# Performance work log

Hardware: AMD Instinct MI355X
Metric: run time of the kernel (lower is better)

Reference implementation:

```python
import jax, jax.numpy as jnp
import numpy as np


def setup_inputs() -> dict:
    key = jax.random.key(0)
    k1, k2, k3, k4 = jax.random.split(key, 4)
    N, E, DIN, DOUT = 16384, 8192, 128, 128
    x = jax.random.normal(k1, (N, DIN), dtype=jnp.float32)
    # sparse binary incidence matrix, avg node degree ~ E * 0.005 ~ 41
    H = (jax.random.uniform(k2, (N, E)) < 0.005).astype(jnp.float32)
    W = jax.random.normal(k3, (DOUT, DIN), dtype=jnp.float32) * (1.0 / np.sqrt(DIN))
    b = jax.random.normal(k4, (DOUT,), dtype=jnp.float32) * 0.01
    return {"x": x, "H": H, "W": W, "b": b}


def reference(x, H, W, b):
    # Degree vectors. Original builds dense diag matrices; off-diagonal zeros
    # raised to negative powers become inf and are zeroed by nan_to_num, so the
    # math reduces to elementwise inverse powers of the degree vectors with
    # non-finite entries mapped to 0.
    deg_node = jnp.sum(H, axis=1)                    # [N]
    deg_edge = jnp.sum(H, axis=0)                    # [E]
    dvih = jnp.where(deg_node > 0, deg_node ** -0.5, 0.0)   # D_v^{-1/2}
    dei = jnp.where(deg_edge > 0, 1.0 / deg_edge, 0.0)      # D_e^{-1}
    # D_v^{-1/2} H D_e^{-1} H^T D_v^{-1/2} x, as broadcasted row scalings
    y = dvih[:, None] * x                            # [N, DIN]
    y = H.T @ y                                      # [E, DIN]
    y = dei[:, None] * y                             # [E, DIN]
    y = H @ y                                        # [N, DIN]
    y = dvih[:, None] * y                            # [N, DIN]
    return y @ W.T + b                               # [N, DOUT]
```

## Files before the change

kernel.cpp:

```cpp
#include <hip/hip_runtime.h>
#include <hip/hip_bf16.h>

#define NN 16384
#define EE 8192
#define DD 128
#define CSR_STRIDE 128
#define CSC_STRIDE 192


__global__ __launch_bounds__(256) void g_gemm(
    const float* __restrict__ x,
    const float* __restrict__ W,
    float* __restrict__ xw,
    int* __restrict__ edge_cnt)
{
    const int t = threadIdx.x;
    {
        int tid = blockIdx.x * 256 + t;
        if (tid < EE) edge_cnt[tid] = 0;
    }

    __shared__ float sA[32 * 132];
    __shared__ float sW[64 * 132];
    const int m0 = blockIdx.x * 32;

#pragma unroll
    for (int r = 0; r < 16; ++r) {
        int i = t + 256 * r;
        int row = i >> 7, col = i & 127;
        sA[row * 132 + col] = x[(size_t)(m0 + row) * DD + col];
    }

    const int jg = t & 15;
    const int mg = t >> 4;
    const int m2 = mg * 2;
    const int j4 = jg * 4;

    for (int h = 0; h < 2; ++h) {
        __syncthreads();
#pragma unroll
        for (int r = 0; r < 32; ++r) {
            int i = t + 256 * r;
            int row = i >> 7, col = i & 127;
            sW[row * 132 + col] = W[(size_t)(h * 64 + row) * DD + col];
        }
        __syncthreads();

        float acc0[4] = {0.f, 0.f, 0.f, 0.f};
        float acc1[4] = {0.f, 0.f, 0.f, 0.f};
#pragma unroll 4
        for (int k = 0; k < 128; k += 4) {
            float4 a0 = *(const float4*)&sA[m2 * 132 + k];
            float4 a1 = *(const float4*)&sA[(m2 + 1) * 132 + k];
#pragma unroll
            for (int jj = 0; jj < 4; ++jj) {
                float4 w = *(const float4*)&sW[(j4 + jj) * 132 + k];
                acc0[jj] += a0.x*w.x + a0.y*w.y + a0.z*w.z + a0.w*w.w;
                acc1[jj] += a1.x*w.x + a1.y*w.y + a1.z*w.z + a1.w*w.w;
            }
        }
#pragma unroll
        for (int jj = 0; jj < 4; ++jj) {
            xw[(size_t)(m0 + m2)     * DD + h * 64 + j4 + jj] = acc0[jj];
            xw[(size_t)(m0 + m2 + 1) * DD + h * 64 + j4 + jj] = acc1[jj];
        }
    }
}

__global__ __launch_bounds__(256) void k1_parse(
    const float* __restrict__ H,
    float* __restrict__ dvih,
    int* __restrict__ csr_cnt,
    int* __restrict__ csr_idx,
    int* __restrict__ edge_cnt,
    int* __restrict__ csc_idx)
{
    const int n = blockIdx.x;
    const int t = threadIdx.x;
    __shared__ int s_cnt;
    __shared__ int s_list[CSR_STRIDE];
    if (t == 0) s_cnt = 0;
    __syncthreads();

    const float4* row = (const float4*)(H + (size_t)n * EE);
#pragma unroll
    for (int j = 0; j < 8; ++j) {
        int idx = t + 256 * j;
        float4 v = row[idx];
        int base = idx * 4;
        if (v.x != 0.0f) { int p = atomicAdd(&s_cnt, 1); if (p < CSR_STRIDE) s_list[p] = base + 0; }
        if (v.y != 0.0f) { int p = atomicAdd(&s_cnt, 1); if (p < CSR_STRIDE) s_list[p] = base + 1; }
        if (v.z != 0.0f) { int p = atomicAdd(&s_cnt, 1); if (p < CSR_STRIDE) s_list[p] = base + 2; }
        if (v.w != 0.0f) { int p = atomicAdd(&s_cnt, 1); if (p < CSR_STRIDE) s_list[p] = base + 3; }
    }
    __syncthreads();

    int cnt = s_cnt; if (cnt > CSR_STRIDE) cnt = CSR_STRIDE;
    if (t < cnt) {
        int e = s_list[t];
        csr_idx[(size_t)n * CSR_STRIDE + t] = e;
        int pos = atomicAdd(&edge_cnt[e], 1);
        if (pos < CSC_STRIDE) csc_idx[(size_t)e * CSC_STRIDE + pos] = n;
    }
    if (t == 0) {
        csr_cnt[n] = cnt;
        dvih[n] = (cnt > 0) ? (1.0f / sqrtf((float)cnt)) : 0.0f;
    }
}

__global__ __launch_bounds__(128) void k2_edge_gather(
    const float* __restrict__ xw,
    const float* __restrict__ dvih,
    const int* __restrict__ edge_cnt,
    const int* __restrict__ csc_idx,
    float* __restrict__ y2)
{
    const int e = blockIdx.x;
    const int t = threadIdx.x;
    __shared__ int   s_lst[CSC_STRIDE];
    __shared__ float s_dv[CSC_STRIDE];

    int cnt = edge_cnt[e];
    int ccnt = cnt > CSC_STRIDE ? CSC_STRIDE : cnt;
    for (int i = t; i < ccnt; i += 128) {
        int n = csc_idx[(size_t)e * CSC_STRIDE + i];
        s_lst[i] = n;
        s_dv[i]  = dvih[n];
    }
    __syncthreads();

    float s = 0.0f;
    int i = 0;
    for (; i + 8 <= ccnt; i += 8) {
        float partial = 0.0f;
#pragma unroll
        for (int u = 0; u < 8; ++u) {
            partial += s_dv[i + u] * xw[(size_t)s_lst[i + u] * DD + t];
        }
        s += partial;
    }
    for (; i < ccnt; ++i) s += s_dv[i] * xw[(size_t)s_lst[i] * DD + t];

    float dei = (cnt > 0) ? (1.0f / (float)cnt) : 0.0f;
    y2[(size_t)e * DD + t] = s * dei;
}

__global__ __launch_bounds__(128) void k3_node_gather(
    const float* __restrict__ y2,
    const float* __restrict__ dvih,
    const int* __restrict__ csr_cnt,
    const int* __restrict__ csr_idx,
    const float* __restrict__ b,
    float* __restrict__ out)
{
    const int n = blockIdx.x;
    const int t = threadIdx.x;
    __shared__ int s_lst[CSR_STRIDE];

    int cnt = csr_cnt[n];
    if (t < cnt) s_lst[t] = csr_idx[(size_t)n * CSR_STRIDE + t];
    __syncthreads();

    float s = 0.0f;
    int i = 0;
    for (; i + 8 <= cnt; i += 8) {
        float partial = 0.0f;
#pragma unroll
        for (int u = 0; u < 8; ++u) {
            partial += y2[(size_t)s_lst[i + u] * DD + t];
        }
        s += partial;
    }
    for (; i < cnt; ++i) s += y2[(size_t)s_lst[i] * DD + t];

    out[(size_t)n * DD + t] = dvih[n] * s + b[t];
}

extern "C" void kernel_launch(void* const* d_in, const int* in_sizes, int n_in,
                              void* d_out, int out_size, void* d_ws, size_t ws_size,
                              hipStream_t stream) {
    const float* x = (const float*)d_in[0];
    const float* H = (const float*)d_in[1];
    const float* W = (const float*)d_in[2];
    const float* b = (const float*)d_in[3];
    float* out = (float*)d_out;

    char* ws = (char*)d_ws;
    float* dvih    = (float*)(ws + 0);
    int*   csr_cnt = (int*)  (ws + 65536);
    int*   edge_cnt= (int*)  (ws + 131072);
    int*   csr_idx = (int*)  (ws + 163840);
    int*   csc_idx = (int*)  (ws + 8552448);
    float* xw      = (float*)(ws + 14843904);
    float* y2      = (float*)(ws + 23232512);

    g_gemm<<<NN / 32, 256, 0, stream>>>(x, W, xw, edge_cnt);
    k1_parse<<<NN, 256, 0, stream>>>(H, dvih, csr_cnt, csr_idx, edge_cnt, csc_idx);
    k2_edge_gather<<<EE, 128, 0, stream>>>(xw, dvih, edge_cnt, csc_idx, y2);
    k3_node_gather<<<NN, 128, 0, stream>>>(y2, dvih, csr_cnt, csr_idx, b, out);
}
```

Baseline: 767.4 us.

## Fuse GEMM into H-parse kernel, nontemporal H loads, two rows per gather block

The x·W GEMM and the H incidence parse now run in one launch, with blocks branching on block index so the GEMM work overlaps the bandwidth-bound scan of H. The edge_cnt zeroing moves to a memset. H rows are read with nontemporal loads to avoid polluting cache. The edge and node gather kernels now handle two rows per 256-thread block. The fused kernel needs the larger shared-memory footprint for every block, which may lower occupancy for the parse blocks.

```diff
diff --git a/kernel.cpp b/kernel.cpp
--- a/kernel.cpp
+++ b/kernel.cpp
@@ -6,126 +6,124 @@
 #define DD 128
 #define CSR_STRIDE 128
 #define CSC_STRIDE 192
-
-
-__global__ __launch_bounds__(256) void g_gemm(
+#define GEMM_BLOCKS 512
+
+typedef float f4 __attribute__((ext_vector_type(4)));
+
+
+__global__ __launch_bounds__(256) void k1_fused(
+    const float* __restrict__ H,
     const float* __restrict__ x,
     const float* __restrict__ W,
     float* __restrict__ xw,
-    int* __restrict__ edge_cnt)
-{
-    const int t = threadIdx.x;
-    {
-        int tid = blockIdx.x * 256 + t;
-        if (tid < EE) edge_cnt[tid] = 0;
-    }
-
-    __shared__ float sA[32 * 132];
-    __shared__ float sW[64 * 132];
-    const int m0 = blockIdx.x * 32;
-
-#pragma unroll
-    for (int r = 0; r < 16; ++r) {
-        int i = t + 256 * r;
-        int row = i >> 7, col = i & 127;
-        sA[row * 132 + col] = x[(size_t)(m0 + row) * DD + col];
-    }
-
-    const int jg = t & 15;
-    const int mg = t >> 4;
-    const int m2 = mg * 2;
-    const int j4 = jg * 4;
-
-    for (int h = 0; h < 2; ++h) {
-        __syncthreads();
-#pragma unroll
-        for (int r = 0; r < 32; ++r) {
-            int i = t + 256 * r;
-            int row = i >> 7, col = i & 127;
-            sW[row * 132 + col] = W[(size_t)(h * 64 + row) * DD + col];
-        }
-        __syncthreads();
-
-        float acc0[4] = {0.f, 0.f, 0.f, 0.f};
-        float acc1[4] = {0.f, 0.f, 0.f, 0.f};
-#pragma unroll 4
-        for (int k = 0; k < 128; k += 4) {
-            float4 a0 = *(const float4*)&sA[m2 * 132 + k];
-            float4 a1 = *(const float4*)&sA[(m2 + 1) * 132 + k];
-#pragma unroll
-            for (int jj = 0; jj < 4; ++jj) {
-                float4 w = *(const float4*)&sW[(j4 + jj) * 132 + k];
-                acc0[jj] += a0.x*w.x + a0.y*w.y + a0.z*w.z + a0.w*w.w;
-                acc1[jj] += a1.x*w.x + a1.y*w.y + a1.z*w.z + a1.w*w.w;
-            }
-        }
-#pragma unroll
-        for (int jj = 0; jj < 4; ++jj) {
-            xw[(size_t)(m0 + m2)     * DD + h * 64 + j4 + jj] = acc0[jj];
-            xw[(size_t)(m0 + m2 + 1) * DD + h * 64 + j4 + jj] = acc1[jj];
-        }
-    }
-}
-
-__global__ __launch_bounds__(256) void k1_parse(
-    const float* __restrict__ H,
     float* __restrict__ dvih,
     int* __restrict__ csr_cnt,
     int* __restrict__ csr_idx,
     int* __restrict__ edge_cnt,
     int* __restrict__ csc_idx)
 {
-    const int n = blockIdx.x;
+    __shared__ float smem[32 * 132 + 64 * 132];
     const int t = threadIdx.x;
-    __shared__ int s_cnt;
-    __shared__ int s_list[CSR_STRIDE];
-    if (t == 0) s_cnt = 0;
-    __syncthreads();
-
-    const float4* row = (const float4*)(H + (size_t)n * EE);
-#pragma unroll
-    for (int j = 0; j < 8; ++j) {
-        int idx = t + 256 * j;
-        float4 v = row[idx];
-        int base = idx * 4;
-        if (v.x != 0.0f) { int p = atomicAdd(&s_cnt, 1); if (p < CSR_STRIDE) s_list[p] = base + 0; }
-        if (v.y != 0.0f) { int p = atomicAdd(&s_cnt, 1); if (p < CSR_STRIDE) s_list[p] = base + 1; }
-        if (v.z != 0.0f) { int p = atomicAdd(&s_cnt, 1); if (p < CSR_STRIDE) s_list[p] = base + 2; }
-        if (v.w != 0.0f) { int p = atomicAdd(&s_cnt, 1); if (p < CSR_STRIDE) s_list[p] = base + 3; }
-    }
-    __syncthreads();
-
-    int cnt = s_cnt; if (cnt > CSR_STRIDE) cnt = CSR_STRIDE;
-    if (t < cnt) {
-        int e = s_list[t];
-        csr_idx[(size_t)n * CSR_STRIDE + t] = e;
-        int pos = atomicAdd(&edge_cnt[e], 1);
-        if (pos < CSC_STRIDE) csc_idx[(size_t)e * CSC_STRIDE + pos] = n;
-    }
-    if (t == 0) {
-        csr_cnt[n] = cnt;
-        dvih[n] = (cnt > 0) ? (1.0f / sqrtf((float)cnt)) : 0.0f;
-    }
-}
-
-__global__ __launch_bounds__(128) void k2_edge_gather(
+
+    if (blockIdx.x < GEMM_BLOCKS) {
+        float* sA = smem;
+        float* sW = smem + 32 * 132;
+        const int m0 = blockIdx.x * 32;
+
+#pragma unroll
+        for (int r = 0; r < 16; ++r) {
+            int i = t + 256 * r;
+            int row = i >> 7, col = i & 127;
+            sA[row * 132 + col] = x[(size_t)(m0 + row) * DD + col];
+        }
+
+        const int jg = t & 15;
+        const int mg = t >> 4;
+        const int m2 = mg * 2;
+        const int j4 = jg * 4;
+
+        for (int h = 0; h < 2; ++h) {
+            __syncthreads();
+#pragma unroll
+            for (int r = 0; r < 32; ++r) {
+                int i = t + 256 * r;
+                int row = i >> 7, col = i & 127;
+                sW[row * 132 + col] = W[(size_t)(h * 64 + row) * DD + col];
+            }
+            __syncthreads();
+
+            float acc0[4] = {0.f, 0.f, 0.f, 0.f};
+            float acc1[4] = {0.f, 0.f, 0.f, 0.f};
+#pragma unroll 4
+            for (int k = 0; k < 128; k += 4) {
+                float4 a0 = *(const float4*)&sA[m2 * 132 + k];
+                float4 a1 = *(const float4*)&sA[(m2 + 1) * 132 + k];
+#pragma unroll
+                for (int jj = 0; jj < 4; ++jj) {
+                    float4 w = *(const float4*)&sW[(j4 + jj) * 132 + k];
+                    acc0[jj] += a0.x*w.x + a0.y*w.y + a0.z*w.z + a0.w*w.w;
+                    acc1[jj] += a1.x*w.x + a1.y*w.y + a1.z*w.z + a1.w*w.w;
+                }
+            }
+#pragma unroll
+            for (int jj = 0; jj < 4; ++jj) {
+                xw[(size_t)(m0 + m2)     * DD + h * 64 + j4 + jj] = acc0[jj];
+                xw[(size_t)(m0 + m2 + 1) * DD + h * 64 + j4 + jj] = acc1[jj];
+            }
+        }
+    } else {
+        const int n = blockIdx.x - GEMM_BLOCKS;
+        int* s_cnt  = (int*)smem;
+        int* s_list = (int*)smem + 4;
+        if (t == 0) *s_cnt = 0;
+        __syncthreads();
+
+        const f4* row = (const f4*)(H + (size_t)n * EE);
+#pragma unroll
+        for (int j = 0; j < 8; ++j) {
+            int idx = t + 256 * j;
+            f4 v = __builtin_nontemporal_load(row + idx);
+            int base = idx * 4;
+            if (v.x != 0.0f) { int p = atomicAdd(s_cnt, 1); if (p < CSR_STRIDE) s_list[p] = base + 0; }
+            if (v.y != 0.0f) { int p = atomicAdd(s_cnt, 1); if (p < CSR_STRIDE) s_list[p] = base + 1; }
+            if (v.z != 0.0f) { int p = atomicAdd(s_cnt, 1); if (p < CSR_STRIDE) s_list[p] = base + 2; }
+            if (v.w != 0.0f) { int p = atomicAdd(s_cnt, 1); if (p < CSR_STRIDE) s_list[p] = base + 3; }
+        }
+        __syncthreads();
+
+        int cnt = *s_cnt; if (cnt > CSR_STRIDE) cnt = CSR_STRIDE;
+        if (t < cnt) {
+            int e = s_list[t];
+            csr_idx[(size_t)n * CSR_STRIDE + t] = e;
+            int pos = atomicAdd(&edge_cnt[e], 1);
+            if (pos < CSC_STRIDE) csc_idx[(size_t)e * CSC_STRIDE + pos] = n;
+        }
+        if (t == 0) {
+            csr_cnt[n] = cnt;
+            dvih[n] = (cnt > 0) ? (1.0f / sqrtf((float)cnt)) : 0.0f;
+        }
+    }
+}
+
+__global__ __launch_bounds__(256) void k2_edge_gather(
     const float* __restrict__ xw,
     const float* __restrict__ dvih,
     const int* __restrict__ edge_cnt,
     const int* __restrict__ csc_idx,
     float* __restrict__ y2)
 {
-    const int e = blockIdx.x;
-    const int t = threadIdx.x;
-    __shared__ int   s_lst[CSC_STRIDE];
-    __shared__ float s_dv[CSC_STRIDE];
+    const int sub = threadIdx.x >> 7;
+    const int t   = threadIdx.x & 127;
+    const int e   = blockIdx.x * 2 + sub;
+    __shared__ int   s_lst[2][CSC_STRIDE];
+    __shared__ float s_dv[2][CSC_STRIDE];
 
     int cnt = edge_cnt[e];
     int ccnt = cnt > CSC_STRIDE ? CSC_STRIDE : cnt;
     for (int i = t; i < ccnt; i += 128) {
         int n = csc_idx[(size_t)e * CSC_STRIDE + i];
-        s_lst[i] = n;
-        s_dv[i]  = dvih[n];
+        s_lst[sub][i] = n;
+        s_dv[sub][i]  = dvih[n];
     }
     __syncthreads();
 
@@ -135,17 +133,17 @@
         float partial = 0.0f;
 #pragma unroll
         for (int u = 0; u < 8; ++u) {
-            partial += s_dv[i + u] * xw[(size_t)s_lst[i + u] * DD + t];
+            partial += s_dv[sub][i + u] * xw[(size_t)s_lst[sub][i + u] * DD + t];
         }
         s += partial;
     }
-    for (; i < ccnt; ++i) s += s_dv[i] * xw[(size_t)s_lst[i] * DD + t];
+    for (; i < ccnt; ++i) s += s_dv[sub][i] * xw[(size_t)s_lst[sub][i] * DD + t];
 
     float dei = (cnt > 0) ? (1.0f / (float)cnt) : 0.0f;
     y2[(size_t)e * DD + t] = s * dei;
 }
 
-__global__ __launch_bounds__(128) void k3_node_gather(
+__global__ __launch_bounds__(256) void k3_node_gather(
     const float* __restrict__ y2,
     const float* __restrict__ dvih,
     const int* __restrict__ csr_cnt,
@@ -153,12 +151,13 @@
     const float* __restrict__ b,
     float* __restrict__ out)
 {
-    const int n = blockIdx.x;
-    const int t = threadIdx.x;
-    __shared__ int s_lst[CSR_STRIDE];
+    const int sub = threadIdx.x >> 7;
+    const int t   = threadIdx.x & 127;
+    const int n   = blockIdx.x * 2 + sub;
+    __shared__ int s_lst[2][CSR_STRIDE];
 
     int cnt = csr_cnt[n];
-    if (t < cnt) s_lst[t] = csr_idx[(size_t)n * CSR_STRIDE + t];
+    if (t < cnt) s_lst[sub][t] = csr_idx[(size_t)n * CSR_STRIDE + t];
     __syncthreads();
 
     float s = 0.0f;
@@ -167,11 +166,11 @@
         float partial = 0.0f;
 #pragma unroll
         for (int u = 0; u < 8; ++u) {
-            partial += y2[(size_t)s_lst[i + u] * DD + t];
+            partial += y2[(size_t)s_lst[sub][i + u] * DD + t];
         }
         s += partial;
     }
-    for (; i < cnt; ++i) s += y2[(size_t)s_lst[i] * DD + t];
+    for (; i < cnt; ++i) s += y2[(size_t)s_lst[sub][i] * DD + t];
 
     out[(size_t)n * DD + t] = dvih[n] * s + b[t];
 }
@@ -194,8 +193,10 @@
     float* xw      = (float*)(ws + 14843904);
     float* y2      = (float*)(ws + 23232512);
 
-    g_gemm<<<NN / 32, 256, 0, stream>>>(x, W, xw, edge_cnt);
-    k1_parse<<<NN, 256, 0, stream>>>(H, dvih, csr_cnt, csr_idx, edge_cnt, csc_idx);
-    k2_edge_gather<<<EE, 128, 0, stream>>>(xw, dvih, edge_cnt, csc_idx, y2);
-    k3_node_gather<<<NN, 128, 0, stream>>>(y2, dvih, csr_cnt, csr_idx, b, out);
-}
+    hipMemsetAsync(edge_cnt, 0, EE * sizeof(int), stream);
+
+    k1_fused<<<GEMM_BLOCKS + NN, 256, 0, stream>>>(H, x, W, xw, dvih,
+                                                   csr_cnt, csr_idx, edge_cnt, csc_idx);
+    k2_edge_gather<<<EE / 2, 256, 0, stream>>>(xw, dvih, edge_cnt, csc_idx, y2);
+    k3_node_gather<<<NN / 2, 256, 0, stream>>>(y2, dvih, csr_cnt, csr_idx, b, out);
+}
```

Result: slower. 800.5 us (+4.3%).
